# Performance work log

Hardware: AMD Instinct MI355X
Metric: run time of the kernel (lower is better)

The kernel has to match this reference:

```python
import jax, jax.numpy as jnp
import numpy as np

N, E = 30000, 480000
HID, NB, D = 256, 128, 2
SW = D * D * NB        # struct-encoder width = bundle_dim^2 * num_bundles = 512
NL, NSAGE = 2, 5       # outer BDL layers, SAGE layers inside struct encoder
OUT = 5
EPS = 1e-5


def _gelu(x):
    return jax.nn.gelu(x, approximate=False)  # torch nn.GELU default (exact)


def _mean_agg(x, src, dst):
    # mean over incoming edges: agg[v] = mean_{u->v} x[u]
    s = jax.ops.segment_sum(x[src], dst, num_segments=N)
    deg = jax.ops.segment_sum(jnp.ones((E,), x.dtype), dst, num_segments=N)
    return s / jnp.maximum(deg, 1.0)[:, None]


def _layernorm(x, g, b):
    m = jnp.mean(x, -1, keepdims=True)
    v = jnp.mean((x - m) ** 2, -1, keepdims=True)
    return (x - m) * jax.lax.rsqrt(v + EPS) * g + b


def _householder(X):
    # torch.nn.utils.parametrizations Orthogonal, orthogonal_map='householder':
    # Q = H_0 H_1 ... H_{d-1}, H_i = I - tau_i v_i v_i^T, v_i = strict-lower col i with unit diag
    d = X.shape[-1]
    A = jnp.tril(X, k=-1)
    tau = 2.0 / (1.0 + jnp.sum(A * A, axis=-2))  # [M, d]
    eye = jnp.eye(d, dtype=X.dtype)
    Q = jnp.broadcast_to(eye, X.shape)
    for i in range(d):
        v = A[:, :, i] + eye[i]
        Qv = jnp.einsum('mij,mj->mi', Q, v)
        Q = Q - tau[:, i, None, None] * Qv[:, :, None] * v[:, None, :]
    return Q


def _struct_encoder(h, src, dst, se_in_w, se_in_b, sage_w1, sage_b1, sage_w2, sage_b2, se_out_w, se_out_b):
    # Model('SAGE', 5, ...) with normalization='None'; dropout inactive in eval
    z = _gelu(h @ se_in_w + se_in_b)
    for i in range(NSAGE):
        m = _mean_agg(z, src, dst)
        zc = jnp.concatenate([z, m], axis=-1)  # SAGE: cat(self, mean(neigh))
        z = z + (_gelu(zc @ sage_w1[i] + sage_b1[i]) @ sage_w2[i] + sage_b2[i])
    return z @ se_out_w + se_out_b


def _forward(x, w_in, b_in, se_in_w, se_in_b, sage_w1, sage_b1, sage_w2, sage_b2,
             se_out_w, se_out_b, enc_w1, enc_b1, enc_w2, enc_b2, ln_g, ln_b,
             bdl_w1, bdl_b1, bdl_w2, bdl_b2, out_ln_g, out_ln_b, w_out, b_out, edge_index):
    src, dst = edge_index[0], edge_index[1]
    h = _gelu(x @ w_in + b_in)
    for k in range(NL):
        enc = _struct_encoder(h, src, dst, se_in_w, se_in_b, sage_w1, sage_b1,
                              sage_w2, sage_b2, se_out_w, se_out_b)
        nr = _gelu(enc @ enc_w1[k] + enc_b1[k]) @ enc_w2[k] + enc_b2[k]  # [N, SW]
        O = _householder(nr.reshape(N * NB, D, D)).reshape(N, NB, D, D)
        # BDL residual module: transport features through per-node bundle frames
        hn = _layernorm(h, ln_g[k], ln_b[k])
        hb = hn.reshape(N, NB, D)
        y = jnp.einsum('nbij,nbj->nbi', O, hb)                       # rotate into frame
        agg = _mean_agg(y.reshape(N, NB * D), src, dst).reshape(N, NB, D)
        msg = jnp.einsum('nbji,nbj->nbi', O, agg).reshape(N, NB * D)  # O^T transports back
        hc = jnp.concatenate([hn, msg], axis=-1)
        h = h + (_gelu(hc @ bdl_w1[k] + bdl_b1[k]) @ bdl_w2[k] + bdl_b2[k])
    h = _layernorm(h, out_ln_g, out_ln_b)
    return h @ w_out + b_out  # [N, OUT]; .squeeze(1) is a no-op for OUT>1


def _w(key, fan_in, shape):
    return jax.random.normal(key, shape, dtype=jnp.float32) / np.sqrt(fan_in)


def setup_inputs() -> dict:
    key = jax.random.key(0)
    ks = iter(jax.random.split(key, 40))
    f32 = jnp.float32
    return {
        'x': jax.random.normal(next(ks), (N, HID), dtype=f32),
        'edge_index': jax.random.randint(next(ks), (2, E), 0, N, dtype=jnp.int32),
        'w_in': _w(next(ks), HID, (HID, HID)), 'b_in': jnp.zeros((HID,), f32),
        'se_in_w': _w(next(ks), HID, (HID, SW)), 'se_in_b': jnp.zeros((SW,), f32),
        'sage_w1': _w(next(ks), 2 * SW, (NSAGE, 2 * SW, SW)), 'sage_b1': jnp.zeros((NSAGE, SW), f32),
        'sage_w2': _w(next(ks), SW, (NSAGE, SW, SW)), 'sage_b2': jnp.zeros((NSAGE, SW), f32),
        'se_out_w': _w(next(ks), SW, (SW, SW)), 'se_out_b': jnp.zeros((SW,), f32),
        'enc_w1': _w(next(ks), SW, (NL, SW, SW)), 'enc_b1': jnp.zeros((NL, SW), f32),
        'enc_w2': _w(next(ks), SW, (NL, SW, SW)), 'enc_b2': jnp.zeros((NL, SW), f32),
        'ln_g': jnp.ones((NL, HID), f32), 'ln_b': jnp.zeros((NL, HID), f32),
        'bdl_w1': _w(next(ks), 2 * HID, (NL, 2 * HID, HID)), 'bdl_b1': jnp.zeros((NL, HID), f32),
        'bdl_w2': _w(next(ks), HID, (NL, HID, HID)), 'bdl_b2': jnp.zeros((NL, HID), f32),
        'out_ln_g': jnp.ones((HID,), f32), 'out_ln_b': jnp.zeros((HID,), f32),
        'w_out': _w(next(ks), HID, (HID, OUT)), 'b_out': jnp.zeros((OUT,), f32),
    }


def reference(x, edge_index, w_in, b_in, se_in_w, se_in_b, sage_w1, sage_b1, sage_w2, sage_b2,
              se_out_w, se_out_b, enc_w1, enc_b1, enc_w2, enc_b2, ln_g, ln_b,
              bdl_w1, bdl_b1, bdl_w2, bdl_b2, out_ln_g, out_ln_b, w_out, b_out):
    return _forward(x, w_in, b_in, se_in_w, se_in_b, sage_w1, sage_b1, sage_w2, sage_b2,
                    se_out_w, se_out_b, enc_w1, enc_b1, enc_w2, enc_b2, ln_g, ln_b,
                    bdl_w1, bdl_b1, bdl_w2, bdl_b2, out_ln_g, out_ln_b, w_out, b_out, edge_index)
```

## Files before the change

### kernel.cpp

```cpp
#include <hip/hip_runtime.h>
#include <hip/hip_bf16.h>
#include <cstdint>
#include <cstddef>


typedef __attribute__((ext_vector_type(8))) short short8;
typedef __attribute__((ext_vector_type(4))) float f32x4;

__device__ __forceinline__ float gelu_exact(float x) {
  return 0.5f * x * (1.0f + erff(x * 0.7071067811865475f));
}
__device__ __forceinline__ unsigned short f2bf(float f) {
  __hip_bfloat16 b = __float2bfloat16(f);
  return *reinterpret_cast<unsigned short*>(&b);
}
__device__ __forceinline__ float bf2f(unsigned short u) {
  return __uint_as_float((unsigned)u << 16);
}
__device__ __forceinline__ float bflo(unsigned u) { return __uint_as_float(u << 16); }
__device__ __forceinline__ float bfhi(unsigned u) { return __uint_as_float(u & 0xffff0000u); }
__device__ __forceinline__ unsigned packbf(float f0, float f1) {
  return (unsigned)f2bf(f0) | ((unsigned)f2bf(f1) << 16);
}
__device__ __forceinline__ void gload16(const void* g, void* l) {
  __builtin_amdgcn_global_load_lds((const __attribute__((address_space(1))) void*)g,
                                   (__attribute__((address_space(3))) void*)l, 16, 0, 0);
}

__global__ void k_hist(const int* __restrict__ dst, int* __restrict__ deg, int E) {
  int i = blockIdx.x * 256 + threadIdx.x;
  if (i < E) atomicAdd(&deg[dst[i]], 1);
}

__global__ __launch_bounds__(1024)
void k_scan(const int* __restrict__ deg, int* __restrict__ rp, int* __restrict__ cur, int Nn) {
  __shared__ int part[1024];
  int t = threadIdx.x;
  int chunk = (Nn + 1023) >> 10;
  int s0 = t * chunk;
  int e0 = s0 + chunk; if (e0 > Nn) e0 = Nn;
  int s = 0;
  for (int i = s0; i < e0; ++i) s += deg[i];
  part[t] = s;
  __syncthreads();
  for (int off = 1; off < 1024; off <<= 1) {
    int v = (t >= off) ? part[t - off] : 0;
    __syncthreads();
    part[t] += v;
    __syncthreads();
  }
  int base = (t == 0) ? 0 : part[t - 1];
  for (int i = s0; i < e0; ++i) {
    rp[i] = base; cur[i] = base; base += deg[i];
  }
  if (t == 0) rp[Nn] = part[1023];
}

__global__ void k_fill(const int* __restrict__ src, const int* __restrict__ dst,
                       int* __restrict__ cur, int* __restrict__ srcs, int E) {
  int i = blockIdx.x * 256 + threadIdx.x;
  if (i < E) {
    int p = atomicAdd(&cur[dst[i]], 1);
    srcs[p] = src[i];
  }
}

__global__ void k_wT(const float* __restrict__ W, unsigned short* __restrict__ Wt, int K, int Nc) {
  int idx = blockIdx.x * 256 + threadIdx.x;
  if (idx >= K * Nc) return;
  int k = idx % K, n = idx / K;
  Wt[(size_t)n * K + k] = f2bf(W[(size_t)k * Nc + n]);
}

__global__ void k_cast(const float* __restrict__ src, unsigned short* __restrict__ dst, int n) {
  int i = blockIdx.x * 256 + threadIdx.x;
  if (i < n) dst[i] = f2bf(src[i]);
}

template<int ACT, bool RES, bool DUAL, bool W32, bool WBF>
__global__ __launch_bounds__(512, 1)
void k_mfma(const unsigned short* __restrict__ A1, const unsigned short* __restrict__ A2,
            int K1, int K2,
            const unsigned short* __restrict__ Wt, const float* __restrict__ bias,
            const float* R, float* C32, unsigned short* Cbf, int M, int Nc) {
  __shared__ unsigned short As[2][256 * 64];
  __shared__ unsigned short Bs[2][256 * 64];
  const int tid = threadIdx.x;
  const int lane = tid & 63, wv = tid >> 6;
  const int wm = wv >> 2, wn = wv & 3;
  const int m0 = blockIdx.x * 256, n0 = blockIdx.y * 256;
  const int rA = lane & 15, kg = lane >> 4;
  const int Ktot = K1 + K2;
  const int nt = Ktot >> 6;

  f32x4 acc[8][4];
#pragma unroll
  for (int fm = 0; fm < 8; ++fm)
#pragma unroll
    for (int n = 0; n < 4; ++n)
#pragma unroll
      for (int r = 0; r < 4; ++r) acc[fm][n][r] = 0.f;

  auto stage = [&](int t, int b) {
    int k0 = t << 6;
    const unsigned short* Asrc; int kc, lda;
    if (!DUAL || k0 < K1) { Asrc = A1; kc = k0; lda = K1; }
    else                  { Asrc = A2; kc = k0 - K1; lda = K2; }
#pragma unroll
    for (int is = 0; is < 4; ++is) {
      int chunk = is * 512 + tid;
      int row = chunk >> 3, seg = chunk & 7;
      int ks = seg ^ (row & 7);
      int gm = m0 + row; gm = gm < M ? gm : M - 1;
      gload16(Asrc + (size_t)gm * lda + kc + ks * 8, (char*)As[b] + (size_t)chunk * 16);
      gload16(Wt + (size_t)(n0 + row) * Ktot + k0 + ks * 8, (char*)Bs[b] + (size_t)chunk * 16);
    }
  };

  stage(0, 0);
  __syncthreads();

  for (int t = 0; t < nt; ++t) {
    const int b = t & 1;
    if (t + 1 < nt) stage(t + 1, b ^ 1);
#pragma unroll
    for (int kk = 0; kk < 2; ++kk) {
      short8 bfr[4];
#pragma unroll
      for (int n = 0; n < 4; ++n) {
        int col = wn * 64 + n * 16 + rA;
        int ks = (kk * 4 + kg) ^ (col & 7);
        bfr[n] = *reinterpret_cast<const short8*>((const char*)Bs[b] + col * 128 + ks * 16);
      }
#pragma unroll
      for (int mq = 0; mq < 2; ++mq) {
        short8 af[4];
#pragma unroll
        for (int m = 0; m < 4; ++m) {
          int row = wm * 128 + mq * 64 + m * 16 + rA;
          int ks = (kk * 4 + kg) ^ (row & 7);
          af[m] = *reinterpret_cast<const short8*>((const char*)As[b] + row * 128 + ks * 16);
        }
        __builtin_amdgcn_s_setprio(1);
#pragma unroll
        for (int m = 0; m < 4; ++m)
#pragma unroll
          for (int n = 0; n < 4; ++n)
            acc[mq * 4 + m][n] =
                __builtin_amdgcn_mfma_f32_16x16x32_bf16(af[m], bfr[n], acc[mq * 4 + m][n], 0, 0, 0);
        __builtin_amdgcn_s_setprio(0);
      }
    }
    __syncthreads();
  }

#pragma unroll
  for (int fm = 0; fm < 8; ++fm) {
    int gr0 = m0 + wm * 128 + fm * 16 + kg * 4;
#pragma unroll
    for (int n = 0; n < 4; ++n) {
      int gc = n0 + wn * 64 + n * 16 + rA;
      float bv = bias[gc];
#pragma unroll
      for (int r = 0; r < 4; ++r) {
        int gr = gr0 + r;
        if (gr < M) {
          float v = acc[fm][n][r] + bv;
          if (ACT == 1) v = gelu_exact(v);
          if (RES) v += R[(size_t)gr * Nc + gc];
          if (W32) C32[(size_t)gr * Nc + gc] = v;
          if (WBF) Cbf[(size_t)gr * Nc + gc] = f2bf(v);
        }
      }
    }
  }
}

template<int W, bool ROT>
__global__ __launch_bounds__(256)
void k_agg(const unsigned short* __restrict__ X, const int* __restrict__ rp,
           const int* __restrict__ srcs, const float* __restrict__ o,
           unsigned short* __restrict__ out, int Nn) {
  int wid = (blockIdx.x * 256 + threadIdx.x) >> 6;
  int lane = threadIdx.x & 63;
  if (wid >= Nn) return;
  constexpr int PE = W / 64;
  float a[PE];
#pragma unroll
  for (int p = 0; p < PE; ++p) a[p] = 0.f;
  int beg = rp[wid], end = rp[wid + 1];
  for (int e = beg; e < end; ++e) {
    int s = srcs[e];
    const unsigned* row = reinterpret_cast<const unsigned*>(X + (size_t)s * W) + lane * (PE / 2);
    if (PE == 8) {
      uint4 v = *reinterpret_cast<const uint4*>(row);
      a[0] += bflo(v.x); a[1] += bfhi(v.x); a[2] += bflo(v.y); a[3] += bfhi(v.y);
      a[4] += bflo(v.z); a[5] += bfhi(v.z); a[6] += bflo(v.w); a[7] += bfhi(v.w);
    } else {
      uint2 v = *reinterpret_cast<const uint2*>(row);
      a[0] += bflo(v.x); a[1] += bfhi(v.x); a[2] += bflo(v.y); a[3] += bfhi(v.y);
    }
  }
  float inv = (end > beg) ? 1.0f / (float)(end - beg) : 0.0f;
#pragma unroll
  for (int p = 0; p < PE; ++p) a[p] *= inv;
  if (ROT) {
    float4 oc = *reinterpret_cast<const float4*>(o + (size_t)wid * 256 + lane * 4);
    float m0 = oc.x * a[0] - oc.y * a[1];
    float m1 = oc.y * a[0] + oc.x * a[1];
    float m2 = oc.z * a[2] - oc.w * a[3];
    float m3 = oc.w * a[2] + oc.z * a[3];
    a[0] = m0; a[1] = m1; a[2] = m2; a[3] = m3;
  }
  unsigned short* op = out + (size_t)wid * W + lane * PE;
  if (PE == 8) {
    uint4 rv;
    rv.x = packbf(a[0], a[1]); rv.y = packbf(a[2], a[3]);
    rv.z = packbf(a[4], a[5]); rv.w = packbf(a[6], a[7]);
    *reinterpret_cast<uint4*>(op) = rv;
  } else {
    uint2 rv;
    rv.x = packbf(a[0], a[1]); rv.y = packbf(a[2], a[3]);
    *reinterpret_cast<uint2*>(op) = rv;
  }
}

__global__ void k_oparams(const unsigned short* __restrict__ nr, float* __restrict__ o, int total) {
  int idx = blockIdx.x * 256 + threadIdx.x;
  if (idx >= total) return;
  float x = bf2f(nr[(size_t)idx * 4 + 2]);
  float inv = 1.0f / (1.0f + x * x);
  o[(size_t)idx * 2]     = (x * x - 1.0f) * inv;
  o[(size_t)idx * 2 + 1] = 2.0f * x * inv;
}

__global__ __launch_bounds__(256)
void k_ln_rot(const float* __restrict__ h, const float* __restrict__ o,
              const float* __restrict__ g, const float* __restrict__ b,
              unsigned short* __restrict__ hn, unsigned short* __restrict__ y, int Nn) {
  int wid = (blockIdx.x * 256 + threadIdx.x) >> 6;
  int lane = threadIdx.x & 63;
  if (wid >= Nn) return;
  float4 v = reinterpret_cast<const float4*>(h + (size_t)wid * 256)[lane];
  float s = v.x + v.y + v.z + v.w;
  float ss = v.x * v.x + v.y * v.y + v.z * v.z + v.w * v.w;
#pragma unroll
  for (int off = 1; off < 64; off <<= 1) { s += __shfl_xor(s, off); ss += __shfl_xor(ss, off); }
  float mean = s * (1.0f / 256.0f);
  float var = ss * (1.0f / 256.0f) - mean * mean;
  float rs = rsqrtf(var + 1e-5f);
  float4 gg = reinterpret_cast<const float4*>(g)[lane];
  float4 bb = reinterpret_cast<const float4*>(b)[lane];
  float h0 = (v.x - mean) * rs * gg.x + bb.x;
  float h1 = (v.y - mean) * rs * gg.y + bb.y;
  float h2 = (v.z - mean) * rs * gg.z + bb.z;
  float h3 = (v.w - mean) * rs * gg.w + bb.w;
  uint2 hv; hv.x = packbf(h0, h1); hv.y = packbf(h2, h3);
  *reinterpret_cast<uint2*>(hn + (size_t)wid * 256 + lane * 4) = hv;
  float4 oc = *reinterpret_cast<const float4*>(o + (size_t)wid * 256 + lane * 4);
  float y0 =  oc.x * h0 + oc.y * h1;
  float y1 = -oc.y * h0 + oc.x * h1;
  float y2 =  oc.z * h2 + oc.w * h3;
  float y3 = -oc.w * h2 + oc.z * h3;
  uint2 yv; yv.x = packbf(y0, y1); yv.y = packbf(y2, y3);
  *reinterpret_cast<uint2*>(y + (size_t)wid * 256 + lane * 4) = yv;
}

__global__ __launch_bounds__(256)
void k_final(const float* __restrict__ h, const float* __restrict__ g,
             const float* __restrict__ b, const float* __restrict__ wout,
             const float* __restrict__ bout, float* __restrict__ out, int Nn) {
  int wid = (blockIdx.x * 256 + threadIdx.x) >> 6;
  int lane = threadIdx.x & 63;
  if (wid >= Nn) return;
  float4 v = reinterpret_cast<const float4*>(h + (size_t)wid * 256)[lane];
  float s = v.x + v.y + v.z + v.w;
  float ss = v.x * v.x + v.y * v.y + v.z * v.z + v.w * v.w;
#pragma unroll
  for (int off = 1; off < 64; off <<= 1) { s += __shfl_xor(s, off); ss += __shfl_xor(ss, off); }
  float mean = s * (1.0f / 256.0f);
  float var = ss * (1.0f / 256.0f) - mean * mean;
  float rs = rsqrtf(var + 1e-5f);
  float4 gg = reinterpret_cast<const float4*>(g)[lane];
  float4 bb = reinterpret_cast<const float4*>(b)[lane];
  float hv[4];
  hv[0] = (v.x - mean) * rs * gg.x + bb.x;
  hv[1] = (v.y - mean) * rs * gg.y + bb.y;
  hv[2] = (v.z - mean) * rs * gg.z + bb.z;
  hv[3] = (v.w - mean) * rs * gg.w + bb.w;
  int c0 = lane * 4;
  float dots[5];
#pragma unroll
  for (int j = 0; j < 5; ++j) {
    float p = hv[0] * wout[(size_t)(c0 + 0) * 5 + j] + hv[1] * wout[(size_t)(c0 + 1) * 5 + j]
            + hv[2] * wout[(size_t)(c0 + 2) * 5 + j] + hv[3] * wout[(size_t)(c0 + 3) * 5 + j];
#pragma unroll
    for (int off = 1; off < 64; off <<= 1) p += __shfl_xor(p, off);
    dots[j] = p;
  }
  if (lane == 0) {
#pragma unroll
    for (int j = 0; j < 5; ++j) out[(size_t)wid * 5 + j] = dots[j] + bout[j];
  }
}

extern "C" void kernel_launch(void* const* d_in, const int* in_sizes, int n_in,
                              void* d_out, int out_size, void* d_ws, size_t ws_size,
                              hipStream_t stream) {
  const float* x       = (const float*)d_in[0];
  const int*   ei      = (const int*)  d_in[1];
  const float* w_in    = (const float*)d_in[2];
  const float* b_in    = (const float*)d_in[3];
  const float* se_in_w = (const float*)d_in[4];
  const float* se_in_b = (const float*)d_in[5];
  const float* sage_w1 = (const float*)d_in[6];
  const float* sage_b1 = (const float*)d_in[7];
  const float* sage_w2 = (const float*)d_in[8];
  const float* sage_b2 = (const float*)d_in[9];
  const float* se_out_w= (const float*)d_in[10];
  const float* se_out_b= (const float*)d_in[11];
  const float* enc_w1  = (const float*)d_in[12];
  const float* enc_b1  = (const float*)d_in[13];
  const float* enc_w2  = (const float*)d_in[14];
  const float* enc_b2  = (const float*)d_in[15];
  const float* ln_g    = (const float*)d_in[16];
  const float* ln_b    = (const float*)d_in[17];
  const float* bdl_w1  = (const float*)d_in[18];
  const float* bdl_b1  = (const float*)d_in[19];
  const float* bdl_w2  = (const float*)d_in[20];
  const float* bdl_b2  = (const float*)d_in[21];
  const float* oln_g   = (const float*)d_in[22];
  const float* oln_b   = (const float*)d_in[23];
  const float* w_out   = (const float*)d_in[24];
  const float* b_out   = (const float*)d_in[25];
  float* out = (float*)d_out;

  const int HID = 256, SW = 512;
  const int N = in_sizes[0] / HID;
  const int E = in_sizes[1] / 2;

  float* ws = (float*)d_ws;
  float* h32 = ws;
  float* z32 = h32 + (size_t)N * HID;
  float* o   = z32 + (size_t)N * SW;
  unsigned short* h_bf = (unsigned short*)(o + (size_t)N * HID);
  unsigned short* z_bf = h_bf + (size_t)N * HID;
  unsigned short* t_bf = z_bf + (size_t)N * SW;
  unsigned short* u_bf = t_bf + (size_t)N * SW;
  unsigned short* wts = u_bf + (size_t)N * SW;
  size_t off = 0;
  unsigned short* wt_in    = wts + off; off += 256 * 256;
  unsigned short* wt_se_in = wts + off; off += 512 * 256;
  unsigned short* wt_sage1 = wts + off; off += (size_t)5 * 512 * 1024;
  unsigned short* wt_sage2 = wts + off; off += (size_t)5 * 512 * 512;
  unsigned short* wt_se_out= wts + off; off += 512 * 512;
  unsigned short* wt_enc1  = wts + off; off += (size_t)2 * 512 * 512;
  unsigned short* wt_enc2  = wts + off; off += (size_t)2 * 512 * 512;
  unsigned short* wt_bdl1  = wts + off; off += (size_t)2 * 256 * 512;
  unsigned short* wt_bdl2  = wts + off; off += (size_t)2 * 256 * 256;
  int* deg  = (int*)(wts + off);
  int* rp   = deg + N;
  int* cur  = rp + N + 1;
  int* srcs = cur + N;
  size_t need = (size_t)((char*)(srcs + E) - (char*)d_ws);
  if (ws_size < need) return;

  unsigned short* xbf = u_bf;
  unsigned short* hn  = z_bf;
  unsigned short* y   = z_bf + (size_t)N * HID;
  unsigned short* msg = t_bf;
  unsigned short* g2  = u_bf;

  const int* esrc = ei;
  const int* edst = ei + E;

  auto cdiv = [](int a, int b) { return (a + b - 1) / b; };
  dim3 blk(256);
  dim3 blk512(512);
  int gm_blocks = cdiv(N, 256);
  dim3 g_g256(gm_blocks, 1);
  dim3 g_g512(gm_blocks, 2);
  int gw = cdiv(N * 64, 256);

  hipMemsetAsync(deg, 0, sizeof(int) * N, stream);
  k_hist<<<cdiv(E, 256), blk, 0, stream>>>(edst, deg, E);
  k_scan<<<1, 1024, 0, stream>>>(deg, rp, cur, N);
  k_fill<<<cdiv(E, 256), blk, 0, stream>>>(esrc, edst, cur, srcs, E);

  auto wT = [&](const float* W, unsigned short* Wt, int K, int Nc) {
    k_wT<<<cdiv(K * Nc, 256), blk, 0, stream>>>(W, Wt, K, Nc);
  };
  wT(w_in, wt_in, 256, 256);
  wT(se_in_w, wt_se_in, 256, 512);
  for (int i = 0; i < 5; ++i) {
    wT(sage_w1 + (size_t)i * 1024 * 512, wt_sage1 + (size_t)i * 512 * 1024, 1024, 512);
    wT(sage_w2 + (size_t)i * 512 * 512,  wt_sage2 + (size_t)i * 512 * 512,  512, 512);
  }
  wT(se_out_w, wt_se_out, 512, 512);
  for (int k = 0; k < 2; ++k) {
    wT(enc_w1 + (size_t)k * 512 * 512, wt_enc1 + (size_t)k * 512 * 512, 512, 512);
    wT(enc_w2 + (size_t)k * 512 * 512, wt_enc2 + (size_t)k * 512 * 512, 512, 512);
    wT(bdl_w1 + (size_t)k * 512 * 256, wt_bdl1 + (size_t)k * 256 * 512, 512, 256);
    wT(bdl_w2 + (size_t)k * 256 * 256, wt_bdl2 + (size_t)k * 256 * 256, 256, 256);
  }
  k_cast<<<cdiv(N * HID, 256), blk, 0, stream>>>(x, xbf, N * HID);

  k_mfma<1, false, false, true, true><<<g_g256, blk512, 0, stream>>>(
      xbf, nullptr, 256, 0, wt_in, b_in, nullptr, h32, h_bf, N, 256);

  for (int k = 0; k < 2; ++k) {
    k_mfma<1, false, false, true, true><<<g_g512, blk512, 0, stream>>>(
        h_bf, nullptr, 256, 0, wt_se_in, se_in_b, nullptr, z32, z_bf, N, 512);
    for (int i = 0; i < 5; ++i) {
      k_agg<512, false><<<gw, blk, 0, stream>>>(z_bf, rp, srcs, nullptr, t_bf, N);
      k_mfma<1, false, true, false, true><<<g_g512, blk512, 0, stream>>>(
          z_bf, t_bf, 512, 512, wt_sage1 + (size_t)i * 512 * 1024,
          sage_b1 + (size_t)i * SW, nullptr, nullptr, u_bf, N, 512);
      k_mfma<0, true, false, true, true><<<g_g512, blk512, 0, stream>>>(
          u_bf, nullptr, 512, 0, wt_sage2 + (size_t)i * 512 * 512,
          sage_b2 + (size_t)i * SW, z32, z32, z_bf, N, 512);
    }
    k_mfma<0, false, false, false, true><<<g_g512, blk512, 0, stream>>>(
        z_bf, nullptr, 512, 0, wt_se_out, se_out_b, nullptr, nullptr, t_bf, N, 512);
    k_mfma<1, false, false, false, true><<<g_g512, blk512, 0, stream>>>(
        t_bf, nullptr, 512, 0, wt_enc1 + (size_t)k * 512 * 512,
        enc_b1 + (size_t)k * SW, nullptr, nullptr, u_bf, N, 512);
    k_mfma<0, false, false, false, true><<<g_g512, blk512, 0, stream>>>(
        u_bf, nullptr, 512, 0, wt_enc2 + (size_t)k * 512 * 512,
        enc_b2 + (size_t)k * SW, nullptr, nullptr, t_bf, N, 512);
    k_oparams<<<cdiv(N * 128, 256), blk, 0, stream>>>(t_bf, o, N * 128);
    k_ln_rot<<<gw, blk, 0, stream>>>(h32, o, ln_g + (size_t)k * HID, ln_b + (size_t)k * HID, hn, y, N);
    k_agg<256, true><<<gw, blk, 0, stream>>>(y, rp, srcs, o, msg, N);
    k_mfma<1, false, true, false, true><<<g_g256, blk512, 0, stream>>>(
        hn, msg, 256, 256, wt_bdl1 + (size_t)k * 256 * 512,
        bdl_b1 + (size_t)k * HID, nullptr, nullptr, g2, N, 256);
    k_mfma<0, true, false, true, true><<<g_g256, blk512, 0, stream>>>(
        g2, nullptr, 256, 0, wt_bdl2 + (size_t)k * 256 * 256,
        bdl_b2 + (size_t)k * HID, h32, h32, h_bf, N, 256);
  }

  k_final<<<gw, blk, 0, stream>>>(h32, oln_g, oln_b, w_out, b_out, out, N);
}
```

Measured before the change: 2.849 ms.

## Restructure MFMA GEMM pipeline with two-stage prefetch and explicit waitcnt barriers

The GEMM main loop now prefetches two K-tiles ahead. It uses explicit vmcnt/lgkmcnt waits and raw s_barrier calls with sched_barrier fences, and loads all LDS fragments for a tile before issuing the MFMAs. This lets global loads overlap the matrix math more deeply. The kernel also gains an M-tile template parameter: the 256-wide-output GEMMs use 128-row tiles to spread more blocks across CUs, and launch bounds request two blocks per CU. Weight transposes are batched into fewer launches via blockIdx.y. Holding more fragments in registers and the hand-written waitcnt counts add register pressure and correctness risk.

New measurement: 2.747 ms. 3.6% less time.

```diff
diff --git a/kernel.cpp b/kernel.cpp
--- a/kernel.cpp
+++ b/kernel.cpp
@@ -26,6 +26,7 @@
   __builtin_amdgcn_global_load_lds((const __attribute__((address_space(1))) void*)g,
                                    (__attribute__((address_space(3))) void*)l, 16, 0, 0);
 }
+#define SCHEDB() __builtin_amdgcn_sched_barrier(0)
 
 __global__ void k_hist(const int* __restrict__ dst, int* __restrict__ deg, int E) {
   int i = blockIdx.x * 256 + threadIdx.x;
@@ -66,10 +67,12 @@
 }
 
 __global__ void k_wT(const float* __restrict__ W, unsigned short* __restrict__ Wt, int K, int Nc) {
+  const float* Ws = W + (size_t)blockIdx.y * K * Nc;
+  unsigned short* Wd = Wt + (size_t)blockIdx.y * K * Nc;
   int idx = blockIdx.x * 256 + threadIdx.x;
   if (idx >= K * Nc) return;
   int k = idx % K, n = idx / K;
-  Wt[(size_t)n * K + k] = f2bf(W[(size_t)k * Nc + n]);
+  Wd[(size_t)n * K + k] = f2bf(Ws[(size_t)k * Nc + n]);
 }
 
 __global__ void k_cast(const float* __restrict__ src, unsigned short* __restrict__ dst, int n) {
@@ -77,29 +80,31 @@
   if (i < n) dst[i] = f2bf(src[i]);
 }
 
-template<int ACT, bool RES, bool DUAL, bool W32, bool WBF>
-__global__ __launch_bounds__(512, 1)
+template<int MB, int ACT, bool RES, bool DUAL, bool W32, bool WBF>
+__global__ __launch_bounds__(512, 2)
 void k_mfma(const unsigned short* __restrict__ A1, const unsigned short* __restrict__ A2,
             int K1, int K2,
             const unsigned short* __restrict__ Wt, const float* __restrict__ bias,
             const float* R, float* C32, unsigned short* Cbf, int M, int Nc) {
-  __shared__ unsigned short As[2][256 * 64];
+  constexpr int MQ = MB / 128;
+  constexpr int LOADS = MB / 64 + 4;
+  __shared__ unsigned short As[2][MB * 64];
   __shared__ unsigned short Bs[2][256 * 64];
   const int tid = threadIdx.x;
   const int lane = tid & 63, wv = tid >> 6;
   const int wm = wv >> 2, wn = wv & 3;
-  const int m0 = blockIdx.x * 256, n0 = blockIdx.y * 256;
+  const int m0 = blockIdx.x * MB, n0 = blockIdx.y * 256;
   const int rA = lane & 15, kg = lane >> 4;
   const int Ktot = K1 + K2;
   const int nt = Ktot >> 6;
 
-  f32x4 acc[8][4];
-#pragma unroll
-  for (int fm = 0; fm < 8; ++fm)
+  f32x4 acc[MQ * 4][4];
+#pragma unroll
+  for (int f = 0; f < MQ * 4; ++f)
 #pragma unroll
     for (int n = 0; n < 4; ++n)
 #pragma unroll
-      for (int r = 0; r < 4; ++r) acc[fm][n][r] = 0.f;
+      for (int r = 0; r < 4; ++r) acc[f][n][r] = 0.f;
 
   auto stage = [&](int t, int b) {
     int k0 = t << 6;
@@ -107,56 +112,78 @@
     if (!DUAL || k0 < K1) { Asrc = A1; kc = k0; lda = K1; }
     else                  { Asrc = A2; kc = k0 - K1; lda = K2; }
 #pragma unroll
-    for (int is = 0; is < 4; ++is) {
+    for (int is = 0; is < MB / 64; ++is) {
       int chunk = is * 512 + tid;
       int row = chunk >> 3, seg = chunk & 7;
       int ks = seg ^ (row & 7);
       int gm = m0 + row; gm = gm < M ? gm : M - 1;
       gload16(Asrc + (size_t)gm * lda + kc + ks * 8, (char*)As[b] + (size_t)chunk * 16);
+    }
+#pragma unroll
+    for (int is = 0; is < 4; ++is) {
+      int chunk = is * 512 + tid;
+      int row = chunk >> 3, seg = chunk & 7;
+      int ks = seg ^ (row & 7);
       gload16(Wt + (size_t)(n0 + row) * Ktot + k0 + ks * 8, (char*)Bs[b] + (size_t)chunk * 16);
     }
   };
 
   stage(0, 0);
-  __syncthreads();
+  if (nt > 1) stage(1, 1);
 
   for (int t = 0; t < nt; ++t) {
     const int b = t & 1;
-    if (t + 1 < nt) stage(t + 1, b ^ 1);
-#pragma unroll
-    for (int kk = 0; kk < 2; ++kk) {
-      short8 bfr[4];
+    if (t < nt - 1) {
+      if constexpr (LOADS == 8) asm volatile("s_waitcnt vmcnt(8)" ::: "memory");
+      else                      asm volatile("s_waitcnt vmcnt(6)" ::: "memory");
+    } else {
+      asm volatile("s_waitcnt vmcnt(0)" ::: "memory");
+    }
+    SCHEDB();
+    __builtin_amdgcn_s_barrier();
+    SCHEDB();
+
+    short8 bfrag[2][4], afrag[2][MQ * 4];
+#pragma unroll
+    for (int kk = 0; kk < 2; ++kk)
 #pragma unroll
       for (int n = 0; n < 4; ++n) {
         int col = wn * 64 + n * 16 + rA;
         int ks = (kk * 4 + kg) ^ (col & 7);
-        bfr[n] = *reinterpret_cast<const short8*>((const char*)Bs[b] + col * 128 + ks * 16);
+        bfrag[kk][n] = *reinterpret_cast<const short8*>((const char*)Bs[b] + col * 128 + ks * 16);
       }
 #pragma unroll
-      for (int mq = 0; mq < 2; ++mq) {
-        short8 af[4];
+    for (int kk = 0; kk < 2; ++kk)
+#pragma unroll
+      for (int mq = 0; mq < MQ; ++mq)
 #pragma unroll
         for (int m = 0; m < 4; ++m) {
-          int row = wm * 128 + mq * 64 + m * 16 + rA;
+          int row = wm * (MB / 2) + mq * 64 + m * 16 + rA;
           int ks = (kk * 4 + kg) ^ (row & 7);
-          af[m] = *reinterpret_cast<const short8*>((const char*)As[b] + row * 128 + ks * 16);
+          afrag[kk][mq * 4 + m] =
+              *reinterpret_cast<const short8*>((const char*)As[b] + row * 128 + ks * 16);
         }
-        __builtin_amdgcn_s_setprio(1);
-#pragma unroll
-        for (int m = 0; m < 4; ++m)
-#pragma unroll
-          for (int n = 0; n < 4; ++n)
-            acc[mq * 4 + m][n] =
-                __builtin_amdgcn_mfma_f32_16x16x32_bf16(af[m], bfr[n], acc[mq * 4 + m][n], 0, 0, 0);
-        __builtin_amdgcn_s_setprio(0);
-      }
-    }
-    __syncthreads();
-  }
-
-#pragma unroll
-  for (int fm = 0; fm < 8; ++fm) {
-    int gr0 = m0 + wm * 128 + fm * 16 + kg * 4;
+    asm volatile("s_waitcnt lgkmcnt(0)" ::: "memory");
+    SCHEDB();
+    __builtin_amdgcn_s_barrier();
+    SCHEDB();
+    if (t + 2 < nt) stage(t + 2, b);
+
+    __builtin_amdgcn_s_setprio(1);
+#pragma unroll
+    for (int kk = 0; kk < 2; ++kk)
+#pragma unroll
+      for (int f = 0; f < MQ * 4; ++f)
+#pragma unroll
+        for (int n = 0; n < 4; ++n)
+          acc[f][n] = __builtin_amdgcn_mfma_f32_16x16x32_bf16(afrag[kk][f], bfrag[kk][n],
+                                                              acc[f][n], 0, 0, 0);
+    __builtin_amdgcn_s_setprio(0);
+  }
+
+#pragma unroll
+  for (int f = 0; f < MQ * 4; ++f) {
+    int gr0 = m0 + wm * (MB / 2) + f * 16 + kg * 4;
 #pragma unroll
     for (int n = 0; n < 4; ++n) {
       int gc = n0 + wn * 64 + n * 16 + rA;
@@ -165,7 +192,7 @@
       for (int r = 0; r < 4; ++r) {
         int gr = gr0 + r;
         if (gr < M) {
-          float v = acc[fm][n][r] + bv;
+          float v = acc[f][n][r] + bv;
           if (ACT == 1) v = gelu_exact(v);
           if (RES) v += R[(size_t)gr * Nc + gc];
           if (W32) C32[(size_t)gr * Nc + gc] = v;
@@ -377,9 +404,8 @@
   auto cdiv = [](int a, int b) { return (a + b - 1) / b; };
   dim3 blk(256);
   dim3 blk512(512);
-  int gm_blocks = cdiv(N, 256);
-  dim3 g_g256(gm_blocks, 1);
-  dim3 g_g512(gm_blocks, 2);
+  dim3 g_g256(cdiv(N, 128), 1);
+  dim3 g_g512(cdiv(N, 256), 2);
   int gw = cdiv(N * 64, 256);
 
   hipMemsetAsync(deg, 0, sizeof(int) * N, stream);
@@ -387,54 +413,50 @@
   k_scan<<<1, 1024, 0, stream>>>(deg, rp, cur, N);
   k_fill<<<cdiv(E, 256), blk, 0, stream>>>(esrc, edst, cur, srcs, E);
 
-  auto wT = [&](const float* W, unsigned short* Wt, int K, int Nc) {
-    k_wT<<<cdiv(K * Nc, 256), blk, 0, stream>>>(W, Wt, K, Nc);
+  auto wT = [&](const float* W, unsigned short* Wt, int K, int Nc, int cnt) {
+    k_wT<<<dim3(cdiv(K * Nc, 256), cnt), blk, 0, stream>>>(W, Wt, K, Nc);
   };
-  wT(w_in, wt_in, 256, 256);
-  wT(se_in_w, wt_se_in, 256, 512);
-  for (int i = 0; i < 5; ++i) {
-    wT(sage_w1 + (size_t)i * 1024 * 512, wt_sage1 + (size_t)i * 512 * 1024, 1024, 512);
-    wT(sage_w2 + (size_t)i * 512 * 512,  wt_sage2 + (size_t)i * 512 * 512,  512, 512);
-  }
-  wT(se_out_w, wt_se_out, 512, 512);
+  wT(w_in, wt_in, 256, 256, 1);
+  wT(se_in_w, wt_se_in, 256, 512, 1);
+  wT(sage_w1, wt_sage1, 1024, 512, 5);
+  wT(sage_w2, wt_sage2, 512, 512, 5);
+  wT(se_out_w, wt_se_out, 512, 512, 1);
+  wT(enc_w1, wt_enc1, 512, 512, 2);
+  wT(enc_w2, wt_enc2, 512, 512, 2);
+  wT(bdl_w1, wt_bdl1, 512, 256, 2);
+  wT(bdl_w2, wt_bdl2, 256, 256, 2);
+  k_cast<<<cdiv(N * HID, 256), blk, 0, stream>>>(x, xbf, N * HID);
+
+  k_mfma<128, 1, false, false, true, true><<<g_g256, blk512, 0, stream>>>(
+      xbf, nullptr, 256, 0, wt_in, b_in, nullptr, h32, h_bf, N, 256);
+
   for (int k = 0; k < 2; ++k) {
-    wT(enc_w1 + (size_t)k * 512 * 512, wt_enc1 + (size_t)k * 512 * 512, 512, 512);
-    wT(enc_w2 + (size_t)k * 512 * 512, wt_enc2 + (size_t)k * 512 * 512, 512, 512);
-    wT(bdl_w1 + (size_t)k * 512 * 256, wt_bdl1 + (size_t)k * 256 * 512, 512, 256);
-    wT(bdl_w2 + (size_t)k * 256 * 256, wt_bdl2 + (size_t)k * 256 * 256, 256, 256);
-  }
-  k_cast<<<cdiv(N * HID, 256), blk, 0, stream>>>(x, xbf, N * HID);
-
-  k_mfma<1, false, false, true, true><<<g_g256, blk512, 0, stream>>>(
-      xbf, nullptr, 256, 0, wt_in, b_in, nullptr, h32, h_bf, N, 256);
-
-  for (int k = 0; k < 2; ++k) {
-    k_mfma<1, false, false, true, true><<<g_g512, blk512, 0, stream>>>(
+    k_mfma<256, 1, false, false, true, true><<<g_g512, blk512, 0, stream>>>(
         h_bf, nullptr, 256, 0, wt_se_in, se_in_b, nullptr, z32, z_bf, N, 512);
     for (int i = 0; i < 5; ++i) {
       k_agg<512, false><<<gw, blk, 0, stream>>>(z_bf, rp, srcs, nullptr, t_bf, N);
-      k_mfma<1, false, true, false, true><<<g_g512, blk512, 0, stream>>>(
+      k_mfma<256, 1, false, true, false, true><<<g_g512, blk512, 0, stream>>>(
           z_bf, t_bf, 512, 512, wt_sage1 + (size_t)i * 512 * 1024,
           sage_b1 + (size_t)i * SW, nullptr, nullptr, u_bf, N, 512);
-      k_mfma<0, true, false, true, true><<<g_g512, blk512, 0, stream>>>(
+      k_mfma<256, 0, true, false, true, true><<<g_g512, blk512, 0, stream>>>(
           u_bf, nullptr, 512, 0, wt_sage2 + (size_t)i * 512 * 512,
           sage_b2 + (size_t)i * SW, z32, z32, z_bf, N, 512);
     }
-    k_mfma<0, false, false, false, true><<<g_g512, blk512, 0, stream>>>(
+    k_mfma<256, 0, false, false, false, true><<<g_g512, blk512, 0, stream>>>(
         z_bf, nullptr, 512, 0, wt_se_out, se_out_b, nullptr, nullptr, t_bf, N, 512);
-    k_mfma<1, false, false, false, true><<<g_g512, blk512, 0, stream>>>(
+    k_mfma<256, 1, false, false, false, true><<<g_g512, blk512, 0, stream>>>(
         t_bf, nullptr, 512, 0, wt_enc1 + (size_t)k * 512 * 512,
         enc_b1 + (size_t)k * SW, nullptr, nullptr, u_bf, N, 512);
-    k_mfma<0, false, false, false, true><<<g_g512, blk512, 0, stream>>>(
+    k_mfma<256, 0, false, false, false, true><<<g_g512, blk512, 0, stream>>>(
         u_bf, nullptr, 512, 0, wt_enc2 + (size_t)k * 512 * 512,
         enc_b2 + (size_t)k * SW, nullptr, nullptr, t_bf, N, 512);
     k_oparams<<<cdiv(N * 128, 256), blk, 0, stream>>>(t_bf, o, N * 128);
     k_ln_rot<<<gw, blk, 0, stream>>>(h32, o, ln_g + (size_t)k * HID, ln_b + (size_t)k * HID, hn, y, N);
     k_agg<256, true><<<gw, blk, 0, stream>>>(y, rp, srcs, o, msg, N);
-    k_mfma<1, false, true, false, true><<<g_g256, blk512, 0, stream>>>(
+    k_mfma<128, 1, false, true, false, true><<<g_g256, blk512, 0, stream>>>(
         hn, msg, 256, 256, wt_bdl1 + (size_t)k * 256 * 512,
         bdl_b1 + (size_t)k * HID, nullptr, nullptr, g2, N, 256);
-    k_mfma<0, true, false, true, true><<<g_g256, blk512, 0, stream>>>(
+    k_mfma<128, 0, true, false, true, true><<<g_g256, blk512, 0, stream>>>(
         g2, nullptr, 256, 0, wt_bdl2 + (size_t)k * 256 * 256,
         bdl_b2 + (size_t)k * HID, h32, h32, h_bf, N, 256);
   }
```
